# Optimization experiments

Hardware: AMD Instinct MI355X
Metric: run time of the kernel (lower is better)

## Reference

```python
import jax, jax.numpy as jnp
import numpy as np

EPS_NORM = 1e-12  # F.normalize eps
EPS_BN = 1e-5     # BatchNorm eps


def setup_inputs() -> dict:
    key = jax.random.key(0)
    ks = jax.random.split(key, 8)
    B, N, P, d = 64, 4, 128, 256  # batch, subgraphs, patches/subgraph, feature_dim
    h = 256                        # hidden2[-1]
    C = 2                          # num_class
    totP = N * P                   # 512 == num_patches
    feat = totP * h                # readout size = 131072

    def w(k, shape, s=0.02):
        return jax.random.normal(k, shape, dtype=jnp.float32) * s

    return {
        "x": jax.random.normal(ks[0], (B, totP, d), dtype=jnp.float32),
        "edge_prior_mask": jax.random.uniform(ks[1], (P, P), dtype=jnp.float32),
        # stage1 GCN layers (Linear stored as [in, out])
        "W1": w(ks[2], (d, h)), "b1": jnp.zeros((h,), jnp.float32),
        "g1": jnp.ones((h,), jnp.float32), "be1": jnp.zeros((h,), jnp.float32),
        "W2": w(ks[3], (h, h)), "b2": jnp.zeros((h,), jnp.float32),
        "g2": jnp.ones((h,), jnp.float32), "be2": jnp.zeros((h,), jnp.float32),
        # mlp_causal
        "Wm1": w(ks[4], (feat, 128), 0.005), "bm1": jnp.zeros((128,), jnp.float32),
        "gm1": jnp.ones((128,), jnp.float32), "bem1": jnp.zeros((128,), jnp.float32),
        "Wm2": w(ks[5], (128, 64)), "bm2": jnp.zeros((64,), jnp.float32),
        "gm2": jnp.ones((64,), jnp.float32), "bem2": jnp.zeros((64,), jnp.float32),
        "Wm3": w(ks[6], (64, C)), "bm3": jnp.zeros((C,), jnp.float32),
    }


def reference(x, edge_prior_mask, W1, b1, g1, be1, W2, b2, g2, be2,
              Wm1, bm1, gm1, bem1, Wm2, bm2, gm2, bem2, Wm3, bm3):
    B, totP, d = x.shape
    P = edge_prior_mask.shape[0]
    N = totP // P

    # ---- dynamic edges: per-subgraph cosine similarity * prior mask ----
    xb = x.reshape(B, N, P, d)
    nrm = jnp.linalg.norm(xb, axis=-1, keepdims=True)
    xn = xb / jnp.maximum(nrm, EPS_NORM)
    sim = (jnp.einsum('bnpd,bnqd->bnpq', xn, xn) + 1.0) * 0.5  # [B,N,P,P]
    blocks = sim * edge_prior_mask[None, None]

    # block-diagonal assembly [B, totP, totP]
    edges = jnp.zeros((B, totP, totP), dtype=x.dtype)
    for i in range(N):
        edges = edges.at[:, i * P:(i + 1) * P, i * P:(i + 1) * P].set(blocks[:, i])
    eye = jnp.eye(totP, dtype=x.dtype)
    edges = edges * (1.0 - eye)  # zero the diagonal

    # ---- symmetric degree normalization with self loops ----
    A = edges + eye
    deg = A.sum(-1)  # [B, totP]
    dinv = jnp.where(deg > 0, 1.0 / jnp.sqrt(jnp.maximum(deg, EPS_NORM)), 0.0)
    An = dinv[:, :, None] * A * dinv[:, None, :]

    # ---- two GCN layers: bmm(An, X @ W + b) -> BN (over batch+nodes) -> relu ----
    def bn_relu(hh, g, b):
        m = hh.mean(axis=(0, 1), keepdims=True)
        v = hh.var(axis=(0, 1), keepdims=True)
        return jax.nn.relu(g * (hh - m) / jnp.sqrt(v + EPS_BN) + b)

    h1 = bn_relu(jnp.einsum('bpq,bqh->bph', An, x @ W1 + b1), g1, be1)
    h2 = bn_relu(jnp.einsum('bpq,bqh->bph', An, h1 @ W2 + b2), g2, be2)

    # ---- readout + MLP head (dropout = identity in eval) ----
    graph = h2.reshape(B, -1)

    def bn1d(z, g, b):
        m = z.mean(0, keepdims=True)
        v = z.var(0, keepdims=True)
        return g * (z - m) / jnp.sqrt(v + EPS_BN) + b

    z = jax.nn.relu(bn1d(graph @ Wm1 + bm1, gm1, bem1))
    z = jax.nn.relu(bn1d(z @ Wm2 + bm2, gm2, bem2))
    return z @ Wm3 + bm3
```

## Files before the change

### kernel.cpp

```cpp
#include <hip/hip_runtime.h>
#include <cstdint>
#include <cstddef>

#define P_    128
#define H_    256
#define FEAT_ 131072

__global__ __launch_bounds__(256) void k_xn(
    const float* __restrict__ x, float* __restrict__ xn) {
  const int t = threadIdx.x;
  const int lane = t & 63;
  const int row = blockIdx.x * 4 + (t >> 6);
  const float* xr = x + (size_t)row * 256;
  const float4 v = *(const float4*)(xr + lane * 4);
  float ss = v.x * v.x + v.y * v.y + v.z * v.z + v.w * v.w;
  #pragma unroll
  for (int s = 32; s; s >>= 1) ss += __shfl_xor(ss, s, 64);
  const float inv = 1.0f / fmaxf(sqrtf(ss), 1e-12f);
  *(float4*)(xn + (size_t)row * 256 + lane * 4) =
      make_float4(v.x * inv, v.y * inv, v.z * inv, v.w * inv);
}

__global__ __launch_bounds__(256) void k_simfused(
    const float* __restrict__ xn, const float* __restrict__ mask,
    float* __restrict__ An) {
  __shared__ float Xs[16][128];
  __shared__ float red[128][17];
  __shared__ float dinv_s[128];
  const int blk = blockIdx.x;
  const int t = threadIdx.x;
  const int tp = t >> 4, tq = t & 15;
  const float* Xb = xn + (size_t)blk * (128 * 256);

  float v[8][8];
  #pragma unroll
  for (int i = 0; i < 8; ++i)
    #pragma unroll
    for (int j = 0; j < 8; ++j) v[i][j] = 0.f;

  for (int kc = 0; kc < 16; ++kc) {
    __syncthreads();
    #pragma unroll
    for (int l = 0; l < 2; ++l) {
      const int f = t + 256 * l;
      const int row = f >> 2, k4 = (f & 3) * 4;
      const float4 x4 = *(const float4*)(Xb + (size_t)row * 256 + kc * 16 + k4);
      Xs[k4 + 0][row] = x4.x;
      Xs[k4 + 1][row] = x4.y;
      Xs[k4 + 2][row] = x4.z;
      Xs[k4 + 3][row] = x4.w;
    }
    __syncthreads();
    #pragma unroll
    for (int k = 0; k < 16; ++k) {
      const float4 a0 = *(const float4*)&Xs[k][tp * 8];
      const float4 a1 = *(const float4*)&Xs[k][tp * 8 + 4];
      const float4 b0 = *(const float4*)&Xs[k][tq * 8];
      const float4 b1 = *(const float4*)&Xs[k][tq * 8 + 4];
      const float a[8] = {a0.x, a0.y, a0.z, a0.w, a1.x, a1.y, a1.z, a1.w};
      const float b[8] = {b0.x, b0.y, b0.z, b0.w, b1.x, b1.y, b1.z, b1.w};
      #pragma unroll
      for (int i = 0; i < 8; ++i)
        #pragma unroll
        for (int j = 0; j < 8; ++j) v[i][j] += a[i] * b[j];
    }
  }

  #pragma unroll
  for (int i = 0; i < 8; ++i) {
    const int r = tp * 8 + i;
    const float4 m0 = *(const float4*)(mask + r * 128 + tq * 8);
    const float4 m1 = *(const float4*)(mask + r * 128 + tq * 8 + 4);
    const float mm[8] = {m0.x, m0.y, m0.z, m0.w, m1.x, m1.y, m1.z, m1.w};
    float s = 0.f;
    #pragma unroll
    for (int j = 0; j < 8; ++j) {
      const int c = tq * 8 + j;
      const float vv = (r == c) ? 0.0f : (v[i][j] + 1.0f) * 0.5f * mm[j];
      v[i][j] = vv;
      s += vv;
    }
    red[r][tq] = s;
  }
  __syncthreads();
  if (t < 128) {
    float sm = 0.f;
    #pragma unroll
    for (int u = 0; u < 16; ++u) sm += red[t][u];
    const float deg = 1.0f + sm;
    dinv_s[t] = (deg > 0.0f) ? rsqrtf(fmaxf(deg, 1e-12f)) : 0.0f;
  }
  __syncthreads();

  float dq[8];
  #pragma unroll
  for (int j = 0; j < 8; ++j) dq[j] = dinv_s[tq * 8 + j];
  float* Ab = An + (size_t)blk * 16384;
  #pragma unroll
  for (int i = 0; i < 8; ++i) {
    const int r = tp * 8 + i;
    const float dp = dinv_s[r];
    float o[8];
    #pragma unroll
    for (int j = 0; j < 8; ++j) {
      const int c = tq * 8 + j;
      o[j] = (r == c) ? dp * dq[j] : v[i][j] * dp * dq[j];
    }
    *(float4*)(Ab + (size_t)r * 128 + tq * 8)     = make_float4(o[0], o[1], o[2], o[3]);
    *(float4*)(Ab + (size_t)r * 128 + tq * 8 + 4) = make_float4(o[4], o[5], o[6], o[7]);
  }
}

__global__ __launch_bounds__(256) void k_gemm_t(
    const float* __restrict__ A, const float* __restrict__ W,
    const float* __restrict__ bias, float* __restrict__ out) {
  __shared__ float As[16][64];
  __shared__ float Ws[16][128];
  const int rb = blockIdx.x, cb = blockIdx.y;
  const int t = threadIdx.x, tp = t >> 4, tq = t & 15;
  const int m0 = rb * 64, c0 = cb * 128;

  float acc[4][8];
  #pragma unroll
  for (int j = 0; j < 8; ++j) {
    const int col = c0 + ((j < 4) ? (tq * 4 + j) : (64 + tq * 4 + j - 4));
    const float bj = bias[col];
    #pragma unroll
    for (int i = 0; i < 4; ++i) acc[i][j] = bj;
  }

  for (int kc = 0; kc < 16; ++kc) {
    __syncthreads();
    {
      const int row = t >> 2, k4 = (t & 3) * 4;
      const float4 a4 = *(const float4*)(A + (size_t)(m0 + row) * 256 + kc * 16 + k4);
      As[k4 + 0][row] = a4.x;
      As[k4 + 1][row] = a4.y;
      As[k4 + 2][row] = a4.z;
      As[k4 + 3][row] = a4.w;
    }
    #pragma unroll
    for (int l = 0; l < 2; ++l) {
      const int f = t + 256 * l;
      const int k = f >> 5, c4 = (f & 31) * 4;
      *(float4*)&Ws[k][c4] =
          *(const float4*)(W + (size_t)(kc * 16 + k) * 256 + c0 + c4);
    }
    __syncthreads();
    #pragma unroll
    for (int k = 0; k < 16; ++k) {
      const float4 av = *(const float4*)&As[k][tp * 4];
      const float4 w0 = *(const float4*)&Ws[k][tq * 4];
      const float4 w1 = *(const float4*)&Ws[k][64 + tq * 4];
      const float a[4] = {av.x, av.y, av.z, av.w};
      const float w[8] = {w0.x, w0.y, w0.z, w0.w, w1.x, w1.y, w1.z, w1.w};
      #pragma unroll
      for (int i = 0; i < 4; ++i)
        #pragma unroll
        for (int j = 0; j < 8; ++j) acc[i][j] += a[i] * w[j];
    }
  }

  #pragma unroll
  for (int i = 0; i < 4; ++i) {
    float* orow = out + (size_t)(m0 + tp * 4 + i) * 256 + c0;
    *(float4*)(orow + tq * 4)      = make_float4(acc[i][0], acc[i][1], acc[i][2], acc[i][3]);
    *(float4*)(orow + 64 + tq * 4) = make_float4(acc[i][4], acc[i][5], acc[i][6], acc[i][7]);
  }
}

__global__ __launch_bounds__(256) void k_gemmbn_t(
    const float* __restrict__ A, const float* __restrict__ scsh,
    const float* __restrict__ W, const float* __restrict__ bias,
    float* __restrict__ out) {
  __shared__ float As[16][64];
  __shared__ float Ws[16][128];
  const int rb = blockIdx.x, cb = blockIdx.y;
  const int t = threadIdx.x, tp = t >> 4, tq = t & 15;
  const int m0 = rb * 64, c0 = cb * 128;

  float acc[4][8];
  #pragma unroll
  for (int j = 0; j < 8; ++j) {
    const int col = c0 + ((j < 4) ? (tq * 4 + j) : (64 + tq * 4 + j - 4));
    const float bj = bias[col];
    #pragma unroll
    for (int i = 0; i < 4; ++i) acc[i][j] = bj;
  }

  for (int kc = 0; kc < 16; ++kc) {
    __syncthreads();
    {
      const int row = t >> 2, k4 = (t & 3) * 4;
      const int col = kc * 16 + k4;
      const float4 a4 = *(const float4*)(A + (size_t)(m0 + row) * 256 + col);
      const float4 sc = *(const float4*)(scsh + col);
      const float4 sh = *(const float4*)(scsh + 256 + col);
      As[k4 + 0][row] = fmaxf(a4.x * sc.x + sh.x, 0.0f);
      As[k4 + 1][row] = fmaxf(a4.y * sc.y + sh.y, 0.0f);
      As[k4 + 2][row] = fmaxf(a4.z * sc.z + sh.z, 0.0f);
      As[k4 + 3][row] = fmaxf(a4.w * sc.w + sh.w, 0.0f);
    }
    #pragma unroll
    for (int l = 0; l < 2; ++l) {
      const int f = t + 256 * l;
      const int k = f >> 5, c4 = (f & 31) * 4;
      *(float4*)&Ws[k][c4] =
          *(const float4*)(W + (size_t)(kc * 16 + k) * 256 + c0 + c4);
    }
    __syncthreads();
    #pragma unroll
    for (int k = 0; k < 16; ++k) {
      const float4 av = *(const float4*)&As[k][tp * 4];
      const float4 w0 = *(const float4*)&Ws[k][tq * 4];
      const float4 w1 = *(const float4*)&Ws[k][64 + tq * 4];
      const float a[4] = {av.x, av.y, av.z, av.w};
      const float w[8] = {w0.x, w0.y, w0.z, w0.w, w1.x, w1.y, w1.z, w1.w};
      #pragma unroll
      for (int i = 0; i < 4; ++i)
        #pragma unroll
        for (int j = 0; j < 8; ++j) acc[i][j] += a[i] * w[j];
    }
  }

  #pragma unroll
  for (int i = 0; i < 4; ++i) {
    float* orow = out + (size_t)(m0 + tp * 4 + i) * 256 + c0;
    *(float4*)(orow + tq * 4)      = make_float4(acc[i][0], acc[i][1], acc[i][2], acc[i][3]);
    *(float4*)(orow + 64 + tq * 4) = make_float4(acc[i][4], acc[i][5], acc[i][6], acc[i][7]);
  }
}

__global__ __launch_bounds__(256) void k_bmmst(
    const float* __restrict__ An, const float* __restrict__ XW,
    float* __restrict__ out, float* __restrict__ part) {
  __shared__ float As[16][64];
  __shared__ float Ws[16][128];
  __shared__ float rs[16][128];
  __shared__ float rq[16][128];
  const int blk = blockIdx.x;
  const int y = blockIdx.y;
  const int rh = y >> 1, cb = y & 1;
  const int t = threadIdx.x, tp = t >> 4, tq = t & 15;
  const float* Ab = An + (size_t)blk * 16384 + (size_t)rh * 64 * 128;
  const float* Xb = XW + (size_t)blk * (128 * 256);

  float acc[4][8];
  #pragma unroll
  for (int i = 0; i < 4; ++i)
    #pragma unroll
    for (int j = 0; j < 8; ++j) acc[i][j] = 0.f;

  for (int kc = 0; kc < 8; ++kc) {
    __syncthreads();
    {
      const int row = t >> 2, k4 = (t & 3) * 4;
      const float4 a4 = *(const float4*)(Ab + (size_t)row * 128 + kc * 16 + k4);
      As[k4 + 0][row] = a4.x;
      As[k4 + 1][row] = a4.y;
      As[k4 + 2][row] = a4.z;
      As[k4 + 3][row] = a4.w;
    }
    #pragma unroll
    for (int l = 0; l < 2; ++l) {
      const int f = t + 256 * l;
      const int k = f >> 5, c4 = (f & 31) * 4;
      *(float4*)&Ws[k][c4] =
          *(const float4*)(Xb + (size_t)(kc * 16 + k) * 256 + cb * 128 + c4);
    }
    __syncthreads();
    #pragma unroll
    for (int k = 0; k < 16; ++k) {
      const float4 av = *(const float4*)&As[k][tp * 4];
      const float4 w0 = *(const float4*)&Ws[k][tq * 4];
      const float4 w1 = *(const float4*)&Ws[k][64 + tq * 4];
      const float a[4] = {av.x, av.y, av.z, av.w};
      const float w[8] = {w0.x, w0.y, w0.z, w0.w, w1.x, w1.y, w1.z, w1.w};
      #pragma unroll
      for (int i = 0; i < 4; ++i)
        #pragma unroll
        for (int j = 0; j < 8; ++j) acc[i][j] += a[i] * w[j];
    }
  }

  #pragma unroll
  for (int j = 0; j < 8; ++j) {
    float cs = 0.f, cq = 0.f;
    #pragma unroll
    for (int i = 0; i < 4; ++i) { cs += acc[i][j]; cq += acc[i][j] * acc[i][j]; }
    const int col = (j < 4) ? (tq * 4 + j) : (64 + tq * 4 + j - 4);
    rs[tp][col] = cs;
    rq[tp][col] = cq;
  }
  __syncthreads();
  if (t < 128) {
    float s = 0.f, q = 0.f;
    #pragma unroll
    for (int u = 0; u < 16; ++u) { s += rs[u][t]; q += rq[u][t]; }
    const int base = (blk * 4 + y) * 256;
    part[base + t]       = s;
    part[base + 128 + t] = q;
  }

  #pragma unroll
  for (int i = 0; i < 4; ++i) {
    float* orow = out + (size_t)(blk * 128 + rh * 64 + tp * 4 + i) * 256 + cb * 128;
    *(float4*)(orow + tq * 4)      = make_float4(acc[i][0], acc[i][1], acc[i][2], acc[i][3]);
    *(float4*)(orow + 64 + tq * 4) = make_float4(acc[i][4], acc[i][5], acc[i][6], acc[i][7]);
  }
}

__global__ __launch_bounds__(256) void k_bnscsh(
    const float* __restrict__ part, const float* __restrict__ g,
    const float* __restrict__ be, float* __restrict__ scsh) {
  __shared__ float ss[256], qq[256];
  const int c = blockIdx.x;
  const int cb = c >> 7, lc = c & 127;
  const int u = threadIdx.x;
  const float* p0 = part + (size_t)(u * 4 + cb) * 256;
  const float* p1 = part + (size_t)(u * 4 + 2 + cb) * 256;
  ss[u] = p0[lc] + p1[lc];
  qq[u] = p0[128 + lc] + p1[128 + lc];
  __syncthreads();
  for (int st = 128; st; st >>= 1) {
    if (u < st) { ss[u] += ss[u + st]; qq[u] += qq[u + st]; }
    __syncthreads();
  }
  if (u == 0) {
    const float m = ss[0] * (1.0f / 32768.0f);
    const float var = qq[0] * (1.0f / 32768.0f) - m * m;
    const float sc = g[c] * rsqrtf(var + 1e-5f);
    scsh[c] = sc;
    scsh[256 + c] = be[c] - m * sc;
  }
}

__global__ __launch_bounds__(256) void k_headgemm_v3(
    const float* __restrict__ pre2, const float* __restrict__ scsh,
    const float* __restrict__ Wm1, float* __restrict__ part) {
  __shared__ float graphS[64][128];
  const int t = threadIdx.x;
  const int bid = blockIdx.x;
  const int k0 = bid * 128;
  const int cbase = k0 & 255;

  #pragma unroll
  for (int l = 0; l < 8; ++l) {
    const int f = t + 256 * l;
    const int row = f >> 5, c4 = (f & 31) * 4;
    const float4 p = *(const float4*)(pre2 + (size_t)row * FEAT_ + k0 + c4);
    const float4 sc = *(const float4*)(scsh + cbase + c4);
    const float4 sh = *(const float4*)(scsh + 256 + cbase + c4);
    graphS[row][c4 + 0] = fmaxf(p.x * sc.x + sh.x, 0.0f);
    graphS[row][c4 + 1] = fmaxf(p.y * sc.y + sh.y, 0.0f);
    graphS[row][c4 + 2] = fmaxf(p.z * sc.z + sh.z, 0.0f);
    graphS[row][c4 + 3] = fmaxf(p.w * sc.w + sh.w, 0.0f);
  }
  __syncthreads();

  const int hg = t & 31;
  const int bg = t >> 5;
  float acc[8][4];
  #pragma unroll
  for (int i = 0; i < 8; ++i)
    #pragma unroll
    for (int j = 0; j < 4; ++j) acc[i][j] = 0.f;

  #pragma unroll 2
  for (int kk = 0; kk < 128; kk += 4) {
    const int k = k0 + kk;
    const float4 w0 = *(const float4*)(Wm1 + (size_t)(k + 0) * 128 + hg * 4);
    const float4 w1 = *(const float4*)(Wm1 + (size_t)(k + 1) * 128 + hg * 4);
    const float4 w2 = *(const float4*)(Wm1 + (size_t)(k + 2) * 128 + hg * 4);
    const float4 w3 = *(const float4*)(Wm1 + (size_t)(k + 3) * 128 + hg * 4);
    #pragma unroll
    for (int i = 0; i < 8; ++i) {
      const float4 a = *(const float4*)&graphS[bg * 8 + i][kk];
      acc[i][0] += a.x * w0.x; acc[i][1] += a.x * w0.y;
      acc[i][2] += a.x * w0.z; acc[i][3] += a.x * w0.w;
      acc[i][0] += a.y * w1.x; acc[i][1] += a.y * w1.y;
      acc[i][2] += a.y * w1.z; acc[i][3] += a.y * w1.w;
      acc[i][0] += a.z * w2.x; acc[i][1] += a.z * w2.y;
      acc[i][2] += a.z * w2.z; acc[i][3] += a.z * w2.w;
      acc[i][0] += a.w * w3.x; acc[i][1] += a.w * w3.y;
      acc[i][2] += a.w * w3.z; acc[i][3] += a.w * w3.w;
    }
  }

  float* pb = part + (size_t)bid * 8192;
  #pragma unroll
  for (int i = 0; i < 8; ++i)
    *(float4*)(pb + (bg * 8 + i) * 128 + hg * 4) =
        make_float4(acc[i][0], acc[i][1], acc[i][2], acc[i][3]);
}

__global__ __launch_bounds__(256) void k_headredA(
    const float* __restrict__ part, float* __restrict__ part2) {
  const int o = blockIdx.x * 256 + threadIdx.x;
  const int jg = blockIdx.y;
  const float* base = part + (size_t)jg * 128 * 8192;
  float s = 0.f;
  for (int j = 0; j < 128; ++j) s += base[(size_t)j * 8192 + o];
  part2[(size_t)jg * 8192 + o] = s;
}

__global__ __launch_bounds__(256) void k_headredB(
    const float* __restrict__ part2, float* __restrict__ z1) {
  const int o = blockIdx.x * 256 + threadIdx.x;
  float s = 0.f;
  #pragma unroll
  for (int jg = 0; jg < 8; ++jg) s += part2[(size_t)jg * 8192 + o];
  z1[o] = s;
}

template <int J>
__global__ __launch_bounds__(64) void k_headbn(
    const float* __restrict__ z, const float* __restrict__ g,
    const float* __restrict__ be, float* __restrict__ zr) {
  __shared__ float rs[64], rs2[64];
  const int j = blockIdx.x, b = threadIdx.x;
  const float v = z[b * J + j];
  rs[b] = v; rs2[b] = v * v; __syncthreads();
  for (int s = 32; s; s >>= 1) {
    if (b < s) { rs[b] += rs[b + s]; rs2[b] += rs2[b + s]; }
    __syncthreads();
  }
  const float m = rs[0] * (1.0f / 64.0f);
  const float var = rs2[0] * (1.0f / 64.0f) - m * m;
  const float sc = g[j] * rsqrtf(var + 1e-5f);
  const float sh = be[j] - m * sc;
  zr[b * J + j] = fmaxf(v * sc + sh, 0.0f);
}

__global__ __launch_bounds__(64) void k_headmm2(
    const float* __restrict__ zr1, const float* __restrict__ Wm2,
    float* __restrict__ z2) {
  const int b = blockIdx.x, j = threadIdx.x;
  float acc = 0.f;
  for (int k = 0; k < 128; ++k) acc += zr1[b * 128 + k] * Wm2[k * 64 + j];
  z2[b * 64 + j] = acc;
}

__global__ __launch_bounds__(128) void k_headout(
    const float* __restrict__ zr2, const float* __restrict__ Wm3,
    const float* __restrict__ bm3, float* __restrict__ out) {
  const int t = threadIdx.x;
  const int b = t >> 1, c = t & 1;
  float s = bm3[c];
  for (int k = 0; k < 64; ++k) s += zr2[b * 64 + k] * Wm3[k * 2 + c];
  out[t] = s;
}

extern "C" void kernel_launch(void* const* d_in, const int* in_sizes, int n_in,
                              void* d_out, int out_size, void* d_ws, size_t ws_size,
                              hipStream_t stream) {
  (void)in_sizes; (void)n_in; (void)out_size; (void)ws_size;
  const float* x    = (const float*)d_in[0];
  const float* mask = (const float*)d_in[1];
  const float* W1   = (const float*)d_in[2];
  const float* b1   = (const float*)d_in[3];
  const float* g1   = (const float*)d_in[4];
  const float* be1  = (const float*)d_in[5];
  const float* W2   = (const float*)d_in[6];
  const float* b2   = (const float*)d_in[7];
  const float* g2   = (const float*)d_in[8];
  const float* be2  = (const float*)d_in[9];
  const float* Wm1  = (const float*)d_in[10];
  const float* gm1  = (const float*)d_in[12];
  const float* bem1 = (const float*)d_in[13];
  const float* Wm2  = (const float*)d_in[14];
  const float* gm2  = (const float*)d_in[16];
  const float* bem2 = (const float*)d_in[17];
  const float* Wm3  = (const float*)d_in[18];
  const float* bm3  = (const float*)d_in[19];

  float* ws   = (float*)d_ws;
  float* T1   = ws;
  float* An   = T1 + 8388608;
  float* T2   = An + 4194304;
  float* T3   = T2 + 8388608;
  float* z1   = T3 + 8388608;
  float* dinv = z1 + 8192;
  float* st1  = dinv + 32768;
  float* st2  = st1 + 512;
  float* zr1  = st2 + 512;
  float* z2   = zr1 + 8192;
  float* zr2  = z2 + 4096;

  float* scsh1 = dinv;
  float* scsh2 = dinv + 512;

  k_xn<<<8192, 256, 0, stream>>>(x, T1);
  k_simfused<<<256, 256, 0, stream>>>(T1, mask, An);

  k_gemm_t<<<dim3(512, 2), 256, 0, stream>>>(x, W1, b1, T2);
  k_bmmst<<<dim3(256, 4), 256, 0, stream>>>(An, T2, T3, T1);
  k_bnscsh<<<256, 256, 0, stream>>>(T1, g1, be1, scsh1);

  k_gemmbn_t<<<dim3(512, 2), 256, 0, stream>>>(T3, scsh1, W2, b2, T2);
  k_bmmst<<<dim3(256, 4), 256, 0, stream>>>(An, T2, T3, T1);
  k_bnscsh<<<256, 256, 0, stream>>>(T1, g2, be2, scsh2);

  k_headgemm_v3<<<1024, 256, 0, stream>>>(T3, scsh2, Wm1, T2);
  k_headredA<<<dim3(32, 8), 256, 0, stream>>>(T2, An);
  k_headredB<<<32, 256, 0, stream>>>(An, z1);
  k_headbn<128><<<128, 64, 0, stream>>>(z1, gm1, bem1, zr1);
  k_headmm2<<<64, 64, 0, stream>>>(zr1, Wm2, z2);
  k_headbn<64><<<64, 64, 0, stream>>>(z2, gm2, bem2, zr2);
  k_headout<<<1, 128, 0, stream>>>(zr2, Wm3, bm3, (float*)d_out);
}
```

Baseline: 439.2 us.

## Retile GCN GEMMs to 64-thread blocks with 8x8 micro-tiles and register prefetch

```diff
diff --git a/kernel.cpp b/kernel.cpp
--- a/kernel.cpp
+++ b/kernel.cpp
@@ -111,202 +111,210 @@
   }
 }
 
-__global__ __launch_bounds__(256) void k_gemm_t(
+__global__ __launch_bounds__(64) void k_gemm_t(
     const float* __restrict__ A, const float* __restrict__ W,
     const float* __restrict__ bias, float* __restrict__ out) {
-  __shared__ float As[16][64];
-  __shared__ float Ws[16][128];
-  const int rb = blockIdx.x, cb = blockIdx.y;
-  const int t = threadIdx.x, tp = t >> 4, tq = t & 15;
-  const int m0 = rb * 64, c0 = cb * 128;
-
-  float acc[4][8];
+  __shared__ float As[16][68];
+  __shared__ float Ws[16][68];
+  const int t = threadIdx.x, tp = t >> 3, tq = t & 7;
+  const int m0 = blockIdx.x * 64, c0 = blockIdx.y * 64;
+
+  float acc[8][8];
   #pragma unroll
   for (int j = 0; j < 8; ++j) {
-    const int col = c0 + ((j < 4) ? (tq * 4 + j) : (64 + tq * 4 + j - 4));
-    const float bj = bias[col];
-    #pragma unroll
-    for (int i = 0; i < 4; ++i) acc[i][j] = bj;
+    const int cj = (j < 4) ? (tq * 4 + j) : (32 + tq * 4 + (j - 4));
+    const float bj = bias[c0 + cj];
+    #pragma unroll
+    for (int i = 0; i < 8; ++i) acc[i][j] = bj;
   }
 
   for (int kc = 0; kc < 16; ++kc) {
-    __syncthreads();
-    {
-      const int row = t >> 2, k4 = (t & 3) * 4;
-      const float4 a4 = *(const float4*)(A + (size_t)(m0 + row) * 256 + kc * 16 + k4);
-      As[k4 + 0][row] = a4.x;
-      As[k4 + 1][row] = a4.y;
-      As[k4 + 2][row] = a4.z;
-      As[k4 + 3][row] = a4.w;
-    }
-    #pragma unroll
-    for (int l = 0; l < 2; ++l) {
-      const int f = t + 256 * l;
-      const int k = f >> 5, c4 = (f & 31) * 4;
-      *(float4*)&Ws[k][c4] =
-          *(const float4*)(W + (size_t)(kc * 16 + k) * 256 + c0 + c4);
+    float4 ra[4], rw[4];
+    #pragma unroll
+    for (int l = 0; l < 4; ++l) {
+      ra[l] = *(const float4*)(A + (size_t)(m0 + l * 16 + (t >> 2)) * 256 +
+                               kc * 16 + (t & 3) * 4);
+      rw[l] = *(const float4*)(W + (size_t)(kc * 16 + l * 4 + (t >> 4)) * 256 +
+                               c0 + (t & 15) * 4);
+    }
+    __syncthreads();
+    #pragma unroll
+    for (int l = 0; l < 4; ++l) {
+      const int row = l * 16 + (t >> 2), k4 = (t & 3) * 4;
+      As[k4 + 0][row] = ra[l].x; As[k4 + 1][row] = ra[l].y;
+      As[k4 + 2][row] = ra[l].z; As[k4 + 3][row] = ra[l].w;
+      *(float4*)&Ws[l * 4 + (t >> 4)][(t & 15) * 4] = rw[l];
     }
     __syncthreads();
     #pragma unroll
     for (int k = 0; k < 16; ++k) {
-      const float4 av = *(const float4*)&As[k][tp * 4];
+      const float4 a0 = *(const float4*)&As[k][tp * 4];
+      const float4 a1 = *(const float4*)&As[k][32 + tp * 4];
       const float4 w0 = *(const float4*)&Ws[k][tq * 4];
-      const float4 w1 = *(const float4*)&Ws[k][64 + tq * 4];
-      const float a[4] = {av.x, av.y, av.z, av.w};
+      const float4 w1 = *(const float4*)&Ws[k][32 + tq * 4];
+      const float a[8] = {a0.x, a0.y, a0.z, a0.w, a1.x, a1.y, a1.z, a1.w};
       const float w[8] = {w0.x, w0.y, w0.z, w0.w, w1.x, w1.y, w1.z, w1.w};
       #pragma unroll
-      for (int i = 0; i < 4; ++i)
+      for (int i = 0; i < 8; ++i)
         #pragma unroll
         for (int j = 0; j < 8; ++j) acc[i][j] += a[i] * w[j];
     }
   }
 
   #pragma unroll
-  for (int i = 0; i < 4; ++i) {
-    float* orow = out + (size_t)(m0 + tp * 4 + i) * 256 + c0;
+  for (int i = 0; i < 8; ++i) {
+    const int ri = (i < 4) ? (tp * 4 + i) : (32 + tp * 4 + (i - 4));
+    float* orow = out + (size_t)(m0 + ri) * 256 + c0;
     *(float4*)(orow + tq * 4)      = make_float4(acc[i][0], acc[i][1], acc[i][2], acc[i][3]);
-    *(float4*)(orow + 64 + tq * 4) = make_float4(acc[i][4], acc[i][5], acc[i][6], acc[i][7]);
-  }
-}
-
-__global__ __launch_bounds__(256) void k_gemmbn_t(
+    *(float4*)(orow + 32 + tq * 4) = make_float4(acc[i][4], acc[i][5], acc[i][6], acc[i][7]);
+  }
+}
+
+__global__ __launch_bounds__(64) void k_gemmbn_t(
     const float* __restrict__ A, const float* __restrict__ scsh,
     const float* __restrict__ W, const float* __restrict__ bias,
     float* __restrict__ out) {
-  __shared__ float As[16][64];
-  __shared__ float Ws[16][128];
-  const int rb = blockIdx.x, cb = blockIdx.y;
-  const int t = threadIdx.x, tp = t >> 4, tq = t & 15;
-  const int m0 = rb * 64, c0 = cb * 128;
-
-  float acc[4][8];
+  __shared__ float As[16][68];
+  __shared__ float Ws[16][68];
+  const int t = threadIdx.x, tp = t >> 3, tq = t & 7;
+  const int m0 = blockIdx.x * 64, c0 = blockIdx.y * 64;
+
+  float acc[8][8];
   #pragma unroll
   for (int j = 0; j < 8; ++j) {
-    const int col = c0 + ((j < 4) ? (tq * 4 + j) : (64 + tq * 4 + j - 4));
-    const float bj = bias[col];
-    #pragma unroll
-    for (int i = 0; i < 4; ++i) acc[i][j] = bj;
+    const int cj = (j < 4) ? (tq * 4 + j) : (32 + tq * 4 + (j - 4));
+    const float bj = bias[c0 + cj];
+    #pragma unroll
+    for (int i = 0; i < 8; ++i) acc[i][j] = bj;
   }
 
   for (int kc = 0; kc < 16; ++kc) {
-    __syncthreads();
-    {
-      const int row = t >> 2, k4 = (t & 3) * 4;
-      const int col = kc * 16 + k4;
-      const float4 a4 = *(const float4*)(A + (size_t)(m0 + row) * 256 + col);
-      const float4 sc = *(const float4*)(scsh + col);
-      const float4 sh = *(const float4*)(scsh + 256 + col);
-      As[k4 + 0][row] = fmaxf(a4.x * sc.x + sh.x, 0.0f);
-      As[k4 + 1][row] = fmaxf(a4.y * sc.y + sh.y, 0.0f);
-      As[k4 + 2][row] = fmaxf(a4.z * sc.z + sh.z, 0.0f);
-      As[k4 + 3][row] = fmaxf(a4.w * sc.w + sh.w, 0.0f);
-    }
-    #pragma unroll
-    for (int l = 0; l < 2; ++l) {
-      const int f = t + 256 * l;
-      const int k = f >> 5, c4 = (f & 31) * 4;
-      *(float4*)&Ws[k][c4] =
-          *(const float4*)(W + (size_t)(kc * 16 + k) * 256 + c0 + c4);
+    float4 ra[4], rw[4];
+    const int col = kc * 16 + (t & 3) * 4;
+    const float4 sc = *(const float4*)(scsh + col);
+    const float4 sh = *(const float4*)(scsh + 256 + col);
+    #pragma unroll
+    for (int l = 0; l < 4; ++l) {
+      const float4 p = *(const float4*)(A + (size_t)(m0 + l * 16 + (t >> 2)) * 256 + col);
+      ra[l].x = fmaxf(p.x * sc.x + sh.x, 0.0f);
+      ra[l].y = fmaxf(p.y * sc.y + sh.y, 0.0f);
+      ra[l].z = fmaxf(p.z * sc.z + sh.z, 0.0f);
+      ra[l].w = fmaxf(p.w * sc.w + sh.w, 0.0f);
+      rw[l] = *(const float4*)(W + (size_t)(kc * 16 + l * 4 + (t >> 4)) * 256 +
+                               c0 + (t & 15) * 4);
+    }
+    __syncthreads();
+    #pragma unroll
+    for (int l = 0; l < 4; ++l) {
+      const int row = l * 16 + (t >> 2), k4 = (t & 3) * 4;
+      As[k4 + 0][row] = ra[l].x; As[k4 + 1][row] = ra[l].y;
+      As[k4 + 2][row] = ra[l].z; As[k4 + 3][row] = ra[l].w;
+      *(float4*)&Ws[l * 4 + (t >> 4)][(t & 15) * 4] = rw[l];
     }
     __syncthreads();
     #pragma unroll
     for (int k = 0; k < 16; ++k) {
-      const float4 av = *(const float4*)&As[k][tp * 4];
+      const float4 a0 = *(const float4*)&As[k][tp * 4];
+      const float4 a1 = *(const float4*)&As[k][32 + tp * 4];
       const float4 w0 = *(const float4*)&Ws[k][tq * 4];
-      const float4 w1 = *(const float4*)&Ws[k][64 + tq * 4];
-      const float a[4] = {av.x, av.y, av.z, av.w};
+      const float4 w1 = *(const float4*)&Ws[k][32 + tq * 4];
+      const float a[8] = {a0.x, a0.y, a0.z, a0.w, a1.x, a1.y, a1.z, a1.w};
       const float w[8] = {w0.x, w0.y, w0.z, w0.w, w1.x, w1.y, w1.z, w1.w};
       #pragma unroll
-      for (int i = 0; i < 4; ++i)
+      for (int i = 0; i < 8; ++i)
         #pragma unroll
         for (int j = 0; j < 8; ++j) acc[i][j] += a[i] * w[j];
     }
   }
 
   #pragma unroll
-  for (int i = 0; i < 4; ++i) {
-    float* orow = out + (size_t)(m0 + tp * 4 + i) * 256 + c0;
+  for (int i = 0; i < 8; ++i) {
+    const int ri = (i < 4) ? (tp * 4 + i) : (32 + tp * 4 + (i - 4));
+    float* orow = out + (size_t)(m0 + ri) * 256 + c0;
     *(float4*)(orow + tq * 4)      = make_float4(acc[i][0], acc[i][1], acc[i][2], acc[i][3]);
-    *(float4*)(orow + 64 + tq * 4) = make_float4(acc[i][4], acc[i][5], acc[i][6], acc[i][7]);
-  }
-}
-
-__global__ __launch_bounds__(256) void k_bmmst(
+    *(float4*)(orow + 32 + tq * 4) = make_float4(acc[i][4], acc[i][5], acc[i][6], acc[i][7]);
+  }
+}
+
+__global__ __launch_bounds__(64) void k_bmmst(
     const float* __restrict__ An, const float* __restrict__ XW,
     float* __restrict__ out, float* __restrict__ part) {
-  __shared__ float As[16][64];
-  __shared__ float Ws[16][128];
-  __shared__ float rs[16][128];
-  __shared__ float rq[16][128];
+  __shared__ float As[16][68];
+  __shared__ float Ws[16][68];
+  __shared__ float rs[8][64];
+  __shared__ float rq[8][64];
   const int blk = blockIdx.x;
   const int y = blockIdx.y;
-  const int rh = y >> 1, cb = y & 1;
-  const int t = threadIdx.x, tp = t >> 4, tq = t & 15;
+  const int rh = y >> 2, cq = y & 3;
+  const int t = threadIdx.x, tp = t >> 3, tq = t & 7;
   const float* Ab = An + (size_t)blk * 16384 + (size_t)rh * 64 * 128;
   const float* Xb = XW + (size_t)blk * (128 * 256);
 
-  float acc[4][8];
-  #pragma unroll
-  for (int i = 0; i < 4; ++i)
+  float acc[8][8];
+  #pragma unroll
+  for (int i = 0; i < 8; ++i)
     #pragma unroll
     for (int j = 0; j < 8; ++j) acc[i][j] = 0.f;
 
   for (int kc = 0; kc < 8; ++kc) {
-    __syncthreads();
-    {
-      const int row = t >> 2, k4 = (t & 3) * 4;
-      const float4 a4 = *(const float4*)(Ab + (size_t)row * 128 + kc * 16 + k4);
-      As[k4 + 0][row] = a4.x;
-      As[k4 + 1][row] = a4.y;
-      As[k4 + 2][row] = a4.z;
-      As[k4 + 3][row] = a4.w;
-    }
-    #pragma unroll
-    for (int l = 0; l < 2; ++l) {
-      const int f = t + 256 * l;
-      const int k = f >> 5, c4 = (f & 31) * 4;
-      *(float4*)&Ws[k][c4] =
-          *(const float4*)(Xb + (size_t)(kc * 16 + k) * 256 + cb * 128 + c4);
+    float4 ra[4], rw[4];
+    #pragma unroll
+    for (int l = 0; l < 4; ++l) {
+      ra[l] = *(const float4*)(Ab + (size_t)(l * 16 + (t >> 2)) * 128 +
+                               kc * 16 + (t & 3) * 4);
+      rw[l] = *(const float4*)(Xb + (size_t)(kc * 16 + l * 4 + (t >> 4)) * 256 +
+                               cq * 64 + (t & 15) * 4);
+    }
+    __syncthreads();
+    #pragma unroll
+    for (int l = 0; l < 4; ++l) {
+      const int row = l * 16 + (t >> 2), k4 = (t & 3) * 4;
+      As[k4 + 0][row] = ra[l].x; As[k4 + 1][row] = ra[l].y;
+      As[k4 + 2][row] = ra[l].z; As[k4 + 3][row] = ra[l].w;
+      *(float4*)&Ws[l * 4 + (t >> 4)][(t & 15) * 4] = rw[l];
     }
     __syncthreads();
     #pragma unroll
     for (int k = 0; k < 16; ++k) {
-      const float4 av = *(const float4*)&As[k][tp * 4];
+      const float4 a0 = *(const float4*)&As[k][tp * 4];
+      const float4 a1 = *(const float4*)&As[k][32 + tp * 4];
       const float4 w0 = *(const float4*)&Ws[k][tq * 4];
-      const float4 w1 = *(const float4*)&Ws[k][64 + tq * 4];
-      const float a[4] = {av.x, av.y, av.z, av.w};
+      const float4 w1 = *(const float4*)&Ws[k][32 + tq * 4];
+      const float a[8] = {a0.x, a0.y, a0.z, a0.w, a1.x, a1.y, a1.z, a1.w};
       const float w[8] = {w0.x, w0.y, w0.z, w0.w, w1.x, w1.y, w1.z, w1.w};
       #pragma unroll
-      for (int i = 0; i < 4; ++i)
+      for (int i = 0; i < 8; ++i)
         #pragma unroll
         for (int j = 0; j < 8; ++j) acc[i][j] += a[i] * w[j];
     }
   }
 
+  __syncthreads();
   #pragma unroll
   for (int j = 0; j < 8; ++j) {
-    float cs = 0.f, cq = 0.f;
-    #pragma unroll
-    for (int i = 0; i < 4; ++i) { cs += acc[i][j]; cq += acc[i][j] * acc[i][j]; }
-    const int col = (j < 4) ? (tq * 4 + j) : (64 + tq * 4 + j - 4);
+    const int col = (j < 4) ? (tq * 4 + j) : (32 + tq * 4 + (j - 4));
+    float cs = 0.f, cq2 = 0.f;
+    #pragma unroll
+    for (int i = 0; i < 8; ++i) { cs += acc[i][j]; cq2 += acc[i][j] * acc[i][j]; }
     rs[tp][col] = cs;
-    rq[tp][col] = cq;
+    rq[tp][col] = cq2;
   }
   __syncthreads();
-  if (t < 128) {
+  {
     float s = 0.f, q = 0.f;
     #pragma unroll
-    for (int u = 0; u < 16; ++u) { s += rs[u][t]; q += rq[u][t]; }
-    const int base = (blk * 4 + y) * 256;
-    part[base + t]       = s;
-    part[base + 128 + t] = q;
-  }
-
-  #pragma unroll
-  for (int i = 0; i < 4; ++i) {
-    float* orow = out + (size_t)(blk * 128 + rh * 64 + tp * 4 + i) * 256 + cb * 128;
+    for (int u = 0; u < 8; ++u) { s += rs[u][t]; q += rq[u][t]; }
+    const int base = (blk * 8 + y) * 128;
+    part[base + t]      = s;
+    part[base + 64 + t] = q;
+  }
+
+  #pragma unroll
+  for (int i = 0; i < 8; ++i) {
+    const int ri = (i < 4) ? (tp * 4 + i) : (32 + tp * 4 + (i - 4));
+    float* orow = out + (size_t)(blk * 128 + rh * 64 + ri) * 256 + cq * 64;
     *(float4*)(orow + tq * 4)      = make_float4(acc[i][0], acc[i][1], acc[i][2], acc[i][3]);
-    *(float4*)(orow + 64 + tq * 4) = make_float4(acc[i][4], acc[i][5], acc[i][6], acc[i][7]);
+    *(float4*)(orow + 32 + tq * 4) = make_float4(acc[i][4], acc[i][5], acc[i][6], acc[i][7]);
   }
 }
 
@@ -315,12 +323,12 @@
     const float* __restrict__ be, float* __restrict__ scsh) {
   __shared__ float ss[256], qq[256];
   const int c = blockIdx.x;
-  const int cb = c >> 7, lc = c & 127;
+  const int cqi = c >> 6, lc = c & 63;
   const int u = threadIdx.x;
-  const float* p0 = part + (size_t)(u * 4 + cb) * 256;
-  const float* p1 = part + (size_t)(u * 4 + 2 + cb) * 256;
+  const float* p0 = part + (size_t)(u * 8 + cqi) * 128;
+  const float* p1 = part + (size_t)(u * 8 + 4 + cqi) * 128;
   ss[u] = p0[lc] + p1[lc];
-  qq[u] = p0[128 + lc] + p1[128 + lc];
+  qq[u] = p0[64 + lc] + p1[64 + lc];
   __syncthreads();
   for (int st = 128; st; st >>= 1) {
     if (u < st) { ss[u] += ss[u + st]; qq[u] += qq[u + st]; }
@@ -493,12 +501,12 @@
   k_xn<<<8192, 256, 0, stream>>>(x, T1);
   k_simfused<<<256, 256, 0, stream>>>(T1, mask, An);
 
-  k_gemm_t<<<dim3(512, 2), 256, 0, stream>>>(x, W1, b1, T2);
-  k_bmmst<<<dim3(256, 4), 256, 0, stream>>>(An, T2, T3, T1);
+  k_gemm_t<<<dim3(512, 4), 64, 0, stream>>>(x, W1, b1, T2);
+  k_bmmst<<<dim3(256, 8), 64, 0, stream>>>(An, T2, T3, T1);
   k_bnscsh<<<256, 256, 0, stream>>>(T1, g1, be1, scsh1);
 
-  k_gemmbn_t<<<dim3(512, 2), 256, 0, stream>>>(T3, scsh1, W2, b2, T2);
-  k_bmmst<<<dim3(256, 4), 256, 0, stream>>>(An, T2, T3, T1);
+  k_gemmbn_t<<<dim3(512, 4), 64, 0, stream>>>(T3, scsh1, W2, b2, T2);
+  k_bmmst<<<dim3(256, 8), 64, 0, stream>>>(An, T2, T3, T1);
   k_bnscsh<<<256, 256, 0, stream>>>(T1, g2, be2, scsh2);
 
   k_headgemm_v3<<<1024, 256, 0, stream>>>(T3, scsh2, Wm1, T2);
```

After: 463.2 us. +5.4%, slower.

## Fold row normalization into similarity kernel and fuse MLP head tail

Applied to the files above, without the earlier changes.

```diff
diff --git a/kernel.cpp b/kernel.cpp
--- a/kernel.cpp
+++ b/kernel.cpp
@@ -6,31 +6,18 @@
 #define H_    256
 #define FEAT_ 131072
 
-__global__ __launch_bounds__(256) void k_xn(
-    const float* __restrict__ x, float* __restrict__ xn) {
-  const int t = threadIdx.x;
-  const int lane = t & 63;
-  const int row = blockIdx.x * 4 + (t >> 6);
-  const float* xr = x + (size_t)row * 256;
-  const float4 v = *(const float4*)(xr + lane * 4);
-  float ss = v.x * v.x + v.y * v.y + v.z * v.z + v.w * v.w;
-  #pragma unroll
-  for (int s = 32; s; s >>= 1) ss += __shfl_xor(ss, s, 64);
-  const float inv = 1.0f / fmaxf(sqrtf(ss), 1e-12f);
-  *(float4*)(xn + (size_t)row * 256 + lane * 4) =
-      make_float4(v.x * inv, v.y * inv, v.z * inv, v.w * inv);
-}
-
 __global__ __launch_bounds__(256) void k_simfused(
-    const float* __restrict__ xn, const float* __restrict__ mask,
+    const float* __restrict__ x, const float* __restrict__ mask,
     float* __restrict__ An) {
   __shared__ float Xs[16][128];
   __shared__ float red[128][17];
+  __shared__ float diag_s[128];
+  __shared__ float inv_s[128];
   __shared__ float dinv_s[128];
   const int blk = blockIdx.x;
   const int t = threadIdx.x;
   const int tp = t >> 4, tq = t & 15;
-  const float* Xb = xn + (size_t)blk * (128 * 256);
+  const float* Xb = x + (size_t)blk * (128 * 256);
 
   float v[8][8];
   #pragma unroll
@@ -66,9 +53,22 @@
     }
   }
 
+  if (tp == tq) {
+    #pragma unroll
+    for (int i = 0; i < 8; ++i) diag_s[tp * 8 + i] = v[i][i];
+  }
+  __syncthreads();
+  if (t < 128) inv_s[t] = 1.0f / fmaxf(sqrtf(diag_s[t]), 1e-12f);
+  __syncthreads();
+
+  float ivq[8];
+  #pragma unroll
+  for (int j = 0; j < 8; ++j) ivq[j] = inv_s[tq * 8 + j];
+
   #pragma unroll
   for (int i = 0; i < 8; ++i) {
     const int r = tp * 8 + i;
+    const float ivp = inv_s[r];
     const float4 m0 = *(const float4*)(mask + r * 128 + tq * 8);
     const float4 m1 = *(const float4*)(mask + r * 128 + tq * 8 + 4);
     const float mm[8] = {m0.x, m0.y, m0.z, m0.w, m1.x, m1.y, m1.z, m1.w};
@@ -76,7 +76,8 @@
     #pragma unroll
     for (int j = 0; j < 8; ++j) {
       const int c = tq * 8 + j;
-      const float vv = (r == c) ? 0.0f : (v[i][j] + 1.0f) * 0.5f * mm[j];
+      const float vv = (r == c) ? 0.0f
+                                : (v[i][j] * ivp * ivq[j] + 1.0f) * 0.5f * mm[j];
       v[i][j] = vv;
       s += vv;
     }
@@ -404,51 +405,85 @@
   part2[(size_t)jg * 8192 + o] = s;
 }
 
-__global__ __launch_bounds__(256) void k_headredB(
-    const float* __restrict__ part2, float* __restrict__ z1) {
-  const int o = blockIdx.x * 256 + threadIdx.x;
-  float s = 0.f;
-  #pragma unroll
-  for (int jg = 0; jg < 8; ++jg) s += part2[(size_t)jg * 8192 + o];
-  z1[o] = s;
-}
-
-template <int J>
-__global__ __launch_bounds__(64) void k_headbn(
-    const float* __restrict__ z, const float* __restrict__ g,
-    const float* __restrict__ be, float* __restrict__ zr) {
-  __shared__ float rs[64], rs2[64];
-  const int j = blockIdx.x, b = threadIdx.x;
-  const float v = z[b * J + j];
-  rs[b] = v; rs2[b] = v * v; __syncthreads();
-  for (int s = 32; s; s >>= 1) {
-    if (b < s) { rs[b] += rs[b + s]; rs2[b] += rs2[b + s]; }
-    __syncthreads();
-  }
-  const float m = rs[0] * (1.0f / 64.0f);
-  const float var = rs2[0] * (1.0f / 64.0f) - m * m;
-  const float sc = g[j] * rsqrtf(var + 1e-5f);
-  const float sh = be[j] - m * sc;
-  zr[b * J + j] = fmaxf(v * sc + sh, 0.0f);
-}
-
-__global__ __launch_bounds__(64) void k_headmm2(
-    const float* __restrict__ zr1, const float* __restrict__ Wm2,
-    float* __restrict__ z2) {
-  const int b = blockIdx.x, j = threadIdx.x;
-  float acc = 0.f;
-  for (int k = 0; k < 128; ++k) acc += zr1[b * 128 + k] * Wm2[k * 64 + j];
-  z2[b * 64 + j] = acc;
-}
-
-__global__ __launch_bounds__(128) void k_headout(
-    const float* __restrict__ zr2, const float* __restrict__ Wm3,
-    const float* __restrict__ bm3, float* __restrict__ out) {
+__global__ __launch_bounds__(256) void k_headtail(
+    const float* __restrict__ part2,
+    const float* __restrict__ gm1, const float* __restrict__ bem1,
+    const float* __restrict__ Wm2,
+    const float* __restrict__ gm2, const float* __restrict__ bem2,
+    const float* __restrict__ Wm3, const float* __restrict__ bm3,
+    float* __restrict__ out) {
+  __shared__ float zs[8192];
+  __shared__ float wm2s[8192];
+  __shared__ float zb2[4096];
+  __shared__ float sc1[128], sh1[128], sc2[64], sh2[64];
   const int t = threadIdx.x;
-  const int b = t >> 1, c = t & 1;
-  float s = bm3[c];
-  for (int k = 0; k < 64; ++k) s += zr2[b * 64 + k] * Wm3[k * 2 + c];
-  out[t] = s;
+
+  for (int o = t; o < 8192; o += 256) {
+    float s = 0.f;
+    #pragma unroll
+    for (int jg = 0; jg < 8; ++jg) s += part2[(size_t)jg * 8192 + o];
+    zs[o] = s;
+  }
+  for (int o = t; o < 8192; o += 256) wm2s[o] = Wm2[o];
+  __syncthreads();
+
+  if (t < 128) {
+    float s = 0.f, q = 0.f;
+    for (int b = 0; b < 64; ++b) { const float v = zs[b * 128 + t]; s += v; q += v * v; }
+    const float m = s * (1.0f / 64.0f);
+    const float var = q * (1.0f / 64.0f) - m * m;
+    const float sc = gm1[t] * rsqrtf(var + 1e-5f);
+    sc1[t] = sc; sh1[t] = bem1[t] - m * sc;
+  }
+  __syncthreads();
+  for (int o = t; o < 8192; o += 256)
+    zs[o] = fmaxf(zs[o] * sc1[o & 127] + sh1[o & 127], 0.0f);
+  __syncthreads();
+
+  {
+    const int bq = t >> 4, jq = t & 15;
+    float acc[4][4];
+    #pragma unroll
+    for (int bi = 0; bi < 4; ++bi)
+      #pragma unroll
+      for (int ji = 0; ji < 4; ++ji) acc[bi][ji] = 0.f;
+    for (int k = 0; k < 128; ++k) {
+      const float4 w4 = *(const float4*)&wm2s[k * 64 + jq * 4];
+      const float wv[4] = {w4.x, w4.y, w4.z, w4.w};
+      #pragma unroll
+      for (int bi = 0; bi < 4; ++bi) {
+        const float zv = zs[(bq * 4 + bi) * 128 + k];
+        #pragma unroll
+        for (int ji = 0; ji < 4; ++ji) acc[bi][ji] += zv * wv[ji];
+      }
+    }
+    #pragma unroll
+    for (int bi = 0; bi < 4; ++bi)
+      #pragma unroll
+      for (int ji = 0; ji < 4; ++ji)
+        zb2[(bq * 4 + bi) * 64 + jq * 4 + ji] = acc[bi][ji];
+  }
+  __syncthreads();
+
+  if (t < 64) {
+    float s = 0.f, q = 0.f;
+    for (int b = 0; b < 64; ++b) { const float v = zb2[b * 64 + t]; s += v; q += v * v; }
+    const float m = s * (1.0f / 64.0f);
+    const float var = q * (1.0f / 64.0f) - m * m;
+    const float sc = gm2[t] * rsqrtf(var + 1e-5f);
+    sc2[t] = sc; sh2[t] = bem2[t] - m * sc;
+  }
+  __syncthreads();
+  for (int idx = t; idx < 4096; idx += 256)
+    zb2[idx] = fmaxf(zb2[idx] * sc2[idx & 63] + sh2[idx & 63], 0.0f);
+  __syncthreads();
+
+  if (t < 128) {
+    const int b = t >> 1, c = t & 1;
+    float s = bm3[c];
+    for (int k = 0; k < 64; ++k) s += zb2[b * 64 + k] * Wm3[k * 2 + c];
+    out[t] = s;
+  }
 }
 
 extern "C" void kernel_launch(void* const* d_in, const int* in_sizes, int n_in,
@@ -481,17 +516,12 @@
   float* T3   = T2 + 8388608;
   float* z1   = T3 + 8388608;
   float* dinv = z1 + 8192;
-  float* st1  = dinv + 32768;
-  float* st2  = st1 + 512;
-  float* zr1  = st2 + 512;
-  float* z2   = zr1 + 8192;
-  float* zr2  = z2 + 4096;
+  (void)z1;
 
   float* scsh1 = dinv;
   float* scsh2 = dinv + 512;
 
-  k_xn<<<8192, 256, 0, stream>>>(x, T1);
-  k_simfused<<<256, 256, 0, stream>>>(T1, mask, An);
+  k_simfused<<<256, 256, 0, stream>>>(x, mask, An);
 
   k_gemm_t<<<dim3(512, 2), 256, 0, stream>>>(x, W1, b1, T2);
   k_bmmst<<<dim3(256, 4), 256, 0, stream>>>(An, T2, T3, T1);
@@ -503,9 +533,6 @@
 
   k_headgemm_v3<<<1024, 256, 0, stream>>>(T3, scsh2, Wm1, T2);
   k_headredA<<<dim3(32, 8), 256, 0, stream>>>(T2, An);
-  k_headredB<<<32, 256, 0, stream>>>(An, z1);
-  k_headbn<128><<<128, 64, 0, stream>>>(z1, gm1, bem1, zr1);
-  k_headmm2<<<64, 64, 0, stream>>>(zr1, Wm2, z2);
-  k_headbn<64><<<64, 64, 0, stream>>>(z2, gm2, bem2, zr2);
-  k_headout<<<1, 128, 0, stream>>>(zr2, Wm3, bm3, (float*)d_out);
-}
+  k_headtail<<<1, 256, 0, stream>>>(An, gm1, bem1, Wm2, gm2, bem2,
+                                    Wm3, bm3, (float*)d_out);
+}
```

After: 426.1 us. -3.0%, faster.
